# Performance work log

Hardware: AMD Instinct MI355X
Metric: run time of the kernel (lower is better)

Reference implementation:

```python
import jax, jax.numpy as jnp
import numpy as np

D_MODEL = 1024
NHEAD = 16
DFF = 4096
B = 4
L = 1024
EPS = 1e-5


def _layernorm(x, g, b):
    mu = jnp.mean(x, axis=-1, keepdims=True)
    var = jnp.mean((x - mu) ** 2, axis=-1, keepdims=True)
    return (x - mu) * jax.lax.rsqrt(var + EPS) * g + b


def _mha(q, k, v, wq, bq, wk, bk, wv, bv, wo, bo, mask=None):
    # q: [B,Lq,D], k/v: [B,Lk,D]; weights stored as [D_in, D_out]
    Bq, Lq, D = q.shape
    depth = D // NHEAD

    def split(x):  # [B,L,D] -> [B,H,L,depth]
        return x.reshape(Bq, -1, NHEAD, depth).transpose(0, 2, 1, 3)

    Q = split(q @ wq + bq)
    K = split(k @ wk + bk)
    V = split(v @ wv + bv)
    logits = jnp.einsum('bhqd,bhkd->bhqk', Q, K) / (depth ** 0.5)
    if mask is not None:
        logits = jnp.where(mask, logits, jnp.asarray(-1e9, logits.dtype))
    w = jax.nn.softmax(logits, axis=-1)
    o = jnp.einsum('bhqk,bhkd->bhqd', w, V)
    o = o.transpose(0, 2, 1, 3).reshape(Bq, -1, D)
    return o @ wo + bo


def setup_inputs() -> dict:
    key = jax.random.key(0)
    ks = jax.random.split(key, 16)
    s = 0.02

    def w(k, shp):
        return jax.random.normal(k, shp, jnp.float32) * s

    d, f = D_MODEL, DFF
    inp = {
        'tgt': jax.random.normal(ks[0], (B, L, d), jnp.float32),
        'memory': jax.random.normal(ks[1], (B, L, d), jnp.float32),
        'tgt_mask': jnp.tril(jnp.ones((L, L), jnp.bool_)),
        # self-attention params
        'sa_wq': w(ks[2], (d, d)), 'sa_bq': jnp.zeros((d,), jnp.float32),
        'sa_wk': w(ks[3], (d, d)), 'sa_bk': jnp.zeros((d,), jnp.float32),
        'sa_wv': w(ks[4], (d, d)), 'sa_bv': jnp.zeros((d,), jnp.float32),
        'sa_wo': w(ks[5], (d, d)), 'sa_bo': jnp.zeros((d,), jnp.float32),
        # cross-attention params
        'ca_wq': w(ks[6], (d, d)), 'ca_bq': jnp.zeros((d,), jnp.float32),
        'ca_wk': w(ks[7], (d, d)), 'ca_bk': jnp.zeros((d,), jnp.float32),
        'ca_wv': w(ks[8], (d, d)), 'ca_bv': jnp.zeros((d,), jnp.float32),
        'ca_wo': w(ks[9], (d, d)), 'ca_bo': jnp.zeros((d,), jnp.float32),
        # FFN params
        'ffn_w1': w(ks[10], (d, f)), 'ffn_b1': jnp.zeros((f,), jnp.float32),
        'ffn_w2': w(ks[11], (f, d)), 'ffn_b2': jnp.zeros((d,), jnp.float32),
        # LayerNorm params
        'ln1_g': jnp.ones((d,), jnp.float32), 'ln1_b': jnp.zeros((d,), jnp.float32),
        'ln2_g': jnp.ones((d,), jnp.float32), 'ln2_b': jnp.zeros((d,), jnp.float32),
        'ln3_g': jnp.ones((d,), jnp.float32), 'ln3_b': jnp.zeros((d,), jnp.float32),
    }
    return inp


def reference(tgt, memory, tgt_mask,
              sa_wq, sa_bq, sa_wk, sa_bk, sa_wv, sa_bv, sa_wo, sa_bo,
              ca_wq, ca_bq, ca_wk, ca_bk, ca_wv, ca_bv, ca_wo, ca_bo,
              ffn_w1, ffn_b1, ffn_w2, ffn_b2,
              ln1_g, ln1_b, ln2_g, ln2_b, ln3_g, ln3_b):
    # merge_mask with key_padding_mask=None -> mask used directly, broadcast over B,H
    mask = tgt_mask[None, None, :, :]
    t2 = _mha(tgt, tgt, tgt, sa_wq, sa_bq, sa_wk, sa_bk, sa_wv, sa_bv, sa_wo, sa_bo, mask)
    x = _layernorm(tgt + t2, ln1_g, ln1_b)
    t2 = _mha(x, memory, memory, ca_wq, ca_bq, ca_wk, ca_bk, ca_wv, ca_bv, ca_wo, ca_bo, None)
    x = _layernorm(x + t2, ln2_g, ln2_b)
    t2 = jax.nn.relu(x @ ffn_w1 + ffn_b1) @ ffn_w2 + ffn_b2
    x = _layernorm(x + t2, ln3_g, ln3_b)
    return x
```

## Files before the change

kernel.cpp:

```cpp
#include <hip/hip_runtime.h>
#include <hip/hip_bf16.h>

typedef unsigned short u16;
typedef __attribute__((ext_vector_type(8))) short bf16x8;
typedef __attribute__((ext_vector_type(4))) float floatx4;

__device__ inline float u2f(unsigned u) { union { unsigned i; float f; } x; x.i = u; return x.f; }
__device__ inline float bflo(unsigned p) { return u2f(p << 16); }
__device__ inline float bfhi(unsigned p) { return u2f(p & 0xffff0000u); }
__device__ inline u16 f2bf(float f) {
    union { __hip_bfloat16 h; u16 u; } x;
    x.h = __float2bfloat16(f);
    return x.u;
}
__device__ inline unsigned pk2bf(float lo, float hi) {
    return ((unsigned)f2bf(hi) << 16) | f2bf(lo);
}

#define GLDS(g, l) __builtin_amdgcn_global_load_lds( \
    (const __attribute__((address_space(1))) void*)(g), \
    (__attribute__((address_space(3))) void*)(l), 16, 0, 0)

template<int EPI, int NF>
__global__ __launch_bounds__(256, 2) void gemm_mfma(
        const u16* __restrict__ A, const u16* __restrict__ Bt,
        const float* __restrict__ bias, const u16* __restrict__ res,
        void* __restrict__ Cv, u16* __restrict__ o1, u16* __restrict__ o2,
        int N, int K)
{
    constexpr int BN = NF * 32;
    constexpr int BLOADS = BN / 64;

    __shared__ u16 As0[128 * 32];
    __shared__ u16 Bs0[BN * 32];
    __shared__ u16 As1[128 * 32];
    __shared__ u16 Bs1[BN * 32];
    __shared__ u16 As2[128 * 32];
    __shared__ u16 Bs2[BN * 32];

    const int tid = threadIdx.x;
    const int lane = tid & 63, wv = tid >> 6;
    const int wr = wv >> 1, wc = wv & 1;

    const int gx = gridDim.x;
    const int nwg = gx * gridDim.y;
    const int bid0 = blockIdx.y * gx + blockIdx.x;
    const int nbid = (bid0 & 7) * (nwg >> 3) + (bid0 >> 3);
    const int bx = nbid % gx, by = nbid / gx;
    const int row0 = by * 128, col0 = bx * BN;

    const u16* pa[2];
    int ldst[2];
    #pragma unroll
    for (int i = 0; i < 2; ++i) {
        const int idx = i * 256 + tid;
        const int r = idx >> 2;
        const int kob = (idx & 3) << 4;
        const int sw = kob ^ (((r >> 1) & 3) << 4);
        pa[i] = A + (size_t)(row0 + r) * K + (sw >> 1);
        ldst[i] = idx * 8;
    }
    const u16* pb[BLOADS];
    int ldstB[BLOADS];
    #pragma unroll
    for (int i = 0; i < BLOADS; ++i) {
        const int idx = i * 256 + tid;
        const int r = idx >> 2;
        const int kob = (idx & 3) << 4;
        const int sw = kob ^ (((r >> 1) & 3) << 4);
        pb[i] = Bt + (size_t)(col0 + r) * K + (sw >> 1);
        ldstB[i] = idx * 8;
    }

    int offa[4], offb[NF];
    const int rsel = lane & 15, slot = lane >> 4;
    #pragma unroll
    for (int m = 0; m < 4; ++m) {
        const int ra = wr * 64 + m * 16 + rsel;
        offa[m] = ra * 32 + (((slot << 4) ^ (((ra >> 1) & 3) << 4)) >> 1);
    }
    #pragma unroll
    for (int n = 0; n < NF; ++n) {
        const int rb = wc * (NF * 16) + n * 16 + rsel;
        offb[n] = rb * 32 + (((slot << 4) ^ (((rb >> 1) & 3) << 4)) >> 1);
    }

    floatx4 acc[4][NF] = {};

#define STAGE(AA, BB, t) do {                                   \
        const int ko_ = (t) << 5;                               \
        GLDS(pa[0] + ko_, &AA[ldst[0]]);                        \
        GLDS(pa[1] + ko_, &AA[ldst[1]]);                        \
        _Pragma("unroll")                                       \
        for (int i = 0; i < BLOADS; ++i)                        \
            GLDS(pb[i] + ko_, &BB[ldstB[i]]);                   \
    } while (0)

#define COMPUTE(AA, BB) do {                                    \
        bf16x8 af[4], bfr[NF];                                  \
        _Pragma("unroll")                                       \
        for (int m = 0; m < 4; ++m) af[m] = *(const bf16x8*)&AA[offa[m]]; \
        _Pragma("unroll")                                       \
        for (int n = 0; n < NF; ++n) bfr[n] = *(const bf16x8*)&BB[offb[n]]; \
        _Pragma("unroll")                                       \
        for (int m = 0; m < 4; ++m)                             \
            _Pragma("unroll")                                   \
            for (int n = 0; n < NF; ++n)                        \
                acc[m][n] = __builtin_amdgcn_mfma_f32_16x16x32_bf16( \
                        af[m], bfr[n], acc[m][n], 0, 0, 0);     \
    } while (0)

#define PHASE(CA, CB, NA, NB, t) do {                           \
        if ((t) < nkt - 1) {                                    \
            if constexpr (NF == 4)                              \
                asm volatile("s_waitcnt vmcnt(4)" ::: "memory");\
            else                                                \
                asm volatile("s_waitcnt vmcnt(3)" ::: "memory");\
        } else {                                                \
            asm volatile("s_waitcnt vmcnt(0)" ::: "memory");    \
        }                                                       \
        __builtin_amdgcn_s_barrier();                           \
        __builtin_amdgcn_sched_barrier(0);                      \
        if ((t) + 2 < nkt) STAGE(NA, NB, (t) + 2);              \
        COMPUTE(CA, CB);                                        \
    } while (0)

    const int nkt = K >> 5;
    STAGE(As0, Bs0, 0);
    STAGE(As1, Bs1, 1);
    int t = 0;
    for (; t + 3 <= nkt; t += 3) {
        PHASE(As0, Bs0, As2, Bs2, t);
        PHASE(As1, Bs1, As0, Bs0, t + 1);
        PHASE(As2, Bs2, As1, Bs1, t + 2);
    }
    if (t < nkt)     PHASE(As0, Bs0, As2, Bs2, t);
    if (t + 1 < nkt) PHASE(As1, Bs1, As0, Bs0, t + 1);
#undef STAGE
#undef COMPUTE
#undef PHASE

    const int cr4 = (lane >> 4) * 4;
    const int cc = lane & 15;

    if (EPI == 5 || EPI == 6) {
        const int seg = col0 >> 10;
        const int vtseg = (EPI == 5) ? 2 : 1;
        u16* dst;
        if (EPI == 5) dst = (seg == 0) ? (u16*)Cv : (seg == 1 ? o1 : o2);
        else          dst = (seg == 0) ? (u16*)Cv : o1;

        if (seg == vtseg) {
            #pragma unroll
            for (int n = 0; n < NF; ++n) {
                const int col = col0 + wc * (NF * 16) + n * 16 + cc;
                const float bv = bias[col];
                const int vcol = col & 1023;
                const int h = vcol >> 6, d = vcol & 63;
                #pragma unroll
                for (int m = 0; m < 4; ++m) {
                    const int tk = row0 + wr * 64 + m * 16 + cr4;
                    const int b = tk >> 10;
                    ushort4 o4;
                    o4.x = f2bf(acc[m][n][0] + bv);
                    o4.y = f2bf(acc[m][n][1] + bv);
                    o4.z = f2bf(acc[m][n][2] + bv);
                    o4.w = f2bf(acc[m][n][3] + bv);
                    *(ushort4*)(dst +
                        (((size_t)(b * 16 + h) * 64 + d) * 1024 + (tk & 1023))) = o4;
                }
            }
        } else {
            #pragma unroll
            for (int n = 0; n < NF; ++n) {
                const int col = col0 + wc * (NF * 16) + n * 16 + cc;
                const float bv = bias[col];
                const int oc = col & 1023;
                #pragma unroll
                for (int m = 0; m < 4; ++m) {
                    const int rowb = row0 + wr * 64 + m * 16 + cr4;
                    #pragma unroll
                    for (int r = 0; r < 4; ++r)
                        dst[(size_t)(rowb + r) * 1024 + oc] = f2bf(acc[m][n][r] + bv);
                }
            }
        }
        return;
    }

    #pragma unroll
    for (int n = 0; n < NF; ++n) {
        const int col = col0 + wc * (NF * 16) + n * 16 + cc;
        const float bv = bias[col];
        #pragma unroll
        for (int m = 0; m < 4; ++m) {
            const int rowb = row0 + wr * 64 + m * 16 + cr4;
            #pragma unroll
            for (int r = 0; r < 4; ++r) {
                float v = acc[m][n][r] + bv;
                const size_t o = (size_t)(rowb + r) * N + col;
                if (EPI == 2 || EPI == 3) v += u2f((unsigned)res[o] << 16);
                if (EPI == 1) v = fmaxf(v, 0.f);
                if (EPI == 3) ((float*)Cv)[o] = v;
                else          ((u16*)Cv)[o] = f2bf(v);
            }
        }
    }
}

struct TrwB { const float* w[8]; u16* o[8]; };

__global__ __launch_bounds__(256) void trw8_kernel(TrwB p)
{
    __shared__ float ts[64][65];
    const int tid = threadIdx.x;
    const int n0 = blockIdx.x * 64, k0 = blockIdx.y * 64;
    const float* __restrict__ W = p.w[blockIdx.z];
    u16* __restrict__ Wt = p.o[blockIdx.z];
    const int tr = tid >> 4, tc4 = (tid & 15) * 4;
    #pragma unroll
    for (int i = 0; i < 4; ++i) {
        const float4 v = *(const float4*)(W + (size_t)(k0 + tr + i * 16) * 1024 + n0 + tc4);
        ts[tr + i * 16][tc4 + 0] = v.x;
        ts[tr + i * 16][tc4 + 1] = v.y;
        ts[tr + i * 16][tc4 + 2] = v.z;
        ts[tr + i * 16][tc4 + 3] = v.w;
    }
    __syncthreads();
    #pragma unroll
    for (int i = 0; i < 4; ++i) {
        const int nr = tr + i * 16;
        ushort4 o;
        o.x = f2bf(ts[tc4 + 0][nr]);
        o.y = f2bf(ts[tc4 + 1][nr]);
        o.z = f2bf(ts[tc4 + 2][nr]);
        o.w = f2bf(ts[tc4 + 3][nr]);
        *(ushort4*)(Wt + (size_t)(n0 + nr) * 1024 + k0 + tc4) = o;
    }
}

__global__ __launch_bounds__(256) void trw_kernel(
        const float* __restrict__ W, u16* __restrict__ Wt, int K, int N)
{
    __shared__ float ts[64][65];
    const int tid = threadIdx.x;
    const int n0 = blockIdx.x * 64, k0 = blockIdx.y * 64;
    const int tr = tid >> 4, tc4 = (tid & 15) * 4;
    #pragma unroll
    for (int i = 0; i < 4; ++i) {
        const float4 v = *(const float4*)(W + (size_t)(k0 + tr + i * 16) * N + n0 + tc4);
        ts[tr + i * 16][tc4 + 0] = v.x;
        ts[tr + i * 16][tc4 + 1] = v.y;
        ts[tr + i * 16][tc4 + 2] = v.z;
        ts[tr + i * 16][tc4 + 3] = v.w;
    }
    __syncthreads();
    #pragma unroll
    for (int i = 0; i < 4; ++i) {
        const int nr = tr + i * 16;
        ushort4 o;
        o.x = f2bf(ts[tc4 + 0][nr]);
        o.y = f2bf(ts[tc4 + 1][nr]);
        o.z = f2bf(ts[tc4 + 2][nr]);
        o.w = f2bf(ts[tc4 + 3][nr]);
        *(ushort4*)(Wt + (size_t)(n0 + nr) * K + k0 + tc4) = o;
    }
}

__global__ __launch_bounds__(256) void cvt_kernel(
        const float* __restrict__ in, u16* __restrict__ out, int n4)
{
    for (int i = blockIdx.x * 256 + threadIdx.x; i < n4; i += gridDim.x * 256) {
        const float4 v = ((const float4*)in)[i];
        ushort4 o;
        o.x = f2bf(v.x); o.y = f2bf(v.y); o.z = f2bf(v.z); o.w = f2bf(v.w);
        ((ushort4*)out)[i] = o;
    }
}

__global__ __launch_bounds__(256) void bcat_kernel(
        const float* __restrict__ b0, const float* __restrict__ b1,
        const float* __restrict__ b2, float* __restrict__ o, int n)
{
    const int i = blockIdx.x * 256 + threadIdx.x;
    if (i >= n) return;
    const float* s = (i < 1024) ? b0 : (i < 2048 ? b1 : b2);
    o[i] = s[i & 1023];
}

template<int CAUSAL>
__global__ __launch_bounds__(256) void fattn_mfma(
        const u16* __restrict__ Q, const u16* __restrict__ K,
        const u16* __restrict__ Vt, u16* __restrict__ O)
{
    __shared__ u16 Ks[64 * 64];
    __shared__ u16 Vs[64 * 64];
    __shared__ u16 Ps[64 * 64];

    const int tid = threadIdx.x;
    const int lane = tid & 63, wv = tid >> 6;
    const int g = lane >> 4, qx = lane & 15;
    const int bh = blockIdx.x;
    const int b = bh >> 4, h = bh & 15;
    const int qt = blockIdx.y, q0 = qt * 64;
    const float SCL = 0.18033688011f;

    const size_t qkbase = (size_t)b * (1024 * 1024) + (size_t)h * 64;
    const size_t vtbase = (size_t)bh * 64 * 1024;

    const int qr = wv * 16 + qx;
    const int qg = q0 + qr;
    const int swzq = (qr & 7) << 4;

    bf16x8 qf[2];
    #pragma unroll
    for (int ks = 0; ks < 2; ++ks)
        qf[ks] = *(const bf16x8*)(Q + qkbase + (size_t)qg * 1024 + ks * 32 + g * 8);

    const int r0 = tid >> 3, s0 = tid & 7;

    float m_i = -1e30f, l_i = 0.f;
    floatx4 o_acc[4] = {};

    const int ktmax = CAUSAL ? qt : 15;
    for (int kt = 0; kt <= ktmax; ++kt) {
        __syncthreads();
        #pragma unroll
        for (int i = 0; i < 2; ++i) {
            const int r = i * 32 + r0;
            const uint4 kv = *(const uint4*)(K + qkbase + (size_t)(kt * 64 + r) * 1024 + s0 * 8);
            *(uint4*)((char*)Ks + r * 128 + ((s0 ^ (r & 7)) << 4)) = kv;
            const uint4 vv = *(const uint4*)(Vt + vtbase + (size_t)r * 1024 + kt * 64 + s0 * 8);
            *(uint4*)((char*)Vs + r * 128 + ((s0 ^ (r & 7)) << 4)) = vv;
        }
        __syncthreads();

        floatx4 sa[4] = {};
        #pragma unroll
        for (int ks = 0; ks < 2; ++ks) {
            #pragma unroll
            for (int m = 0; m < 4; ++m) {
                const int rr = m * 16 + qx;
                const int sl = ks * 4 + g;
                const bf16x8 kf = *(const bf16x8*)((char*)Ks + rr * 128 + ((sl ^ (rr & 7)) << 4));
                sa[m] = __builtin_amdgcn_mfma_f32_16x16x32_bf16(kf, qf[ks], sa[m], 0, 0, 0);
            }
        }

        float p[4][4];
        float mx = -1e30f;
        #pragma unroll
        for (int m = 0; m < 4; ++m)
            #pragma unroll
            for (int r = 0; r < 4; ++r) {
                float v = sa[m][r] * SCL;
                if (CAUSAL && kt == qt) {
                    const int kl = m * 16 + g * 4 + r;
                    if (kl > qr) v = -1e30f;
                }
                p[m][r] = v;
                mx = fmaxf(mx, v);
            }
        mx = fmaxf(mx, __shfl_xor(mx, 16));
        mx = fmaxf(mx, __shfl_xor(mx, 32));

        const float mn = fmaxf(m_i, mx);
        const float al = exp2f(m_i - mn);
        m_i = mn;
        float rs = 0.f;
        #pragma unroll
        for (int m = 0; m < 4; ++m)
            #pragma unroll
            for (int r = 0; r < 4; ++r) { p[m][r] = exp2f(p[m][r] - mn); rs += p[m][r]; }
        rs += __shfl_xor(rs, 16);
        rs += __shfl_xor(rs, 32);
        l_i = l_i * al + rs;
        #pragma unroll
        for (int n = 0; n < 4; ++n) o_acc[n] *= al;

        #pragma unroll
        for (int m = 0; m < 4; ++m) {
            uint2 pk;
            pk.x = pk2bf(p[m][0], p[m][1]);
            pk.y = pk2bf(p[m][2], p[m][3]);
            *(uint2*)((char*)Ps + qr * 128 + ((m * 32 + g * 8) ^ swzq)) = pk;
        }

        #pragma unroll
        for (int ks2 = 0; ks2 < 2; ++ks2) {
            const bf16x8 pf = *(const bf16x8*)((char*)Ps + qr * 128 + ((ks2 * 64 + g * 16) ^ swzq));
            #pragma unroll
            for (int n = 0; n < 4; ++n) {
                const int rv = n * 16 + qx;
                const int sl = ks2 * 4 + g;
                const bf16x8 vf = *(const bf16x8*)((char*)Vs + rv * 128 + ((sl ^ (rv & 7)) << 4));
                o_acc[n] = __builtin_amdgcn_mfma_f32_16x16x32_bf16(vf, pf, o_acc[n], 0, 0, 0);
            }
        }
    }

    const float inv = 1.f / l_i;
    #pragma unroll
    for (int n = 0; n < 4; ++n) {
        uint2 ov;
        ov.x = pk2bf(o_acc[n][0] * inv, o_acc[n][1] * inv);
        ov.y = pk2bf(o_acc[n][2] * inv, o_acc[n][3] * inv);
        *(uint2*)((char*)Ps + qr * 128 + ((n * 32 + g * 8) ^ swzq)) = ov;
    }
    const int orow = wv * 16 + (lane >> 2);
    const int swzo = (orow & 7) << 4;
    #pragma unroll
    for (int i = 0; i < 2; ++i) {
        const int cb = ((lane & 3) * 2 + i) * 16;
        const uint4 ov = *(const uint4*)((char*)Ps + orow * 128 + (cb ^ swzo));
        *(uint4*)(O + qkbase + (size_t)(q0 + orow) * 1024 + cb / 2) = ov;
    }
}

__global__ __launch_bounds__(256) void ln_bf16_kernel(
        const u16* __restrict__ X, const float* __restrict__ g,
        const float* __restrict__ bta, u16* __restrict__ Y)
{
    __shared__ float red[4];
    const int row = blockIdx.x, tid = threadIdx.x;
    const int wave = tid >> 6, lane = tid & 63;

    const uint2 u = *(const uint2*)(X + (size_t)row * 1024 + tid * 4);
    const float x0 = bflo(u.x), x1 = bfhi(u.x), x2 = bflo(u.y), x3 = bfhi(u.y);

    float s = x0 + x1 + x2 + x3;
    #pragma unroll
    for (int off = 32; off; off >>= 1) s += __shfl_xor(s, off);
    if (lane == 0) red[wave] = s;
    __syncthreads();
    const float mu = (red[0] + red[1] + red[2] + red[3]) * (1.f / 1024.f);
    __syncthreads();

    const float d0 = x0 - mu, d1 = x1 - mu, d2 = x2 - mu, d3 = x3 - mu;
    float s2 = d0 * d0 + d1 * d1 + d2 * d2 + d3 * d3;
    #pragma unroll
    for (int off = 32; off; off >>= 1) s2 += __shfl_xor(s2, off);
    if (lane == 0) red[wave] = s2;
    __syncthreads();
    const float var = (red[0] + red[1] + red[2] + red[3]) * (1.f / 1024.f);
    const float rs = rsqrtf(var + 1e-5f);

    const float4 gg = ((const float4*)g)[tid];
    const float4 bb = ((const float4*)bta)[tid];
    ushort4 o;
    o.x = f2bf(d0 * rs * gg.x + bb.x);
    o.y = f2bf(d1 * rs * gg.y + bb.y);
    o.z = f2bf(d2 * rs * gg.z + bb.z);
    o.w = f2bf(d3 * rs * gg.w + bb.w);
    *(ushort4*)(Y + (size_t)row * 1024 + tid * 4) = o;
}

__global__ __launch_bounds__(256) void ln_kernel(
        const float* X, const float* __restrict__ g,
        const float* __restrict__ bta, float* Y)
{
    __shared__ float red[4];
    const int row = blockIdx.x;
    const int tid = threadIdx.x;
    const int wave = tid >> 6, lane = tid & 63;

    const float4 v = ((const float4*)(X + (size_t)row * 1024))[tid];

    float s = v.x + v.y + v.z + v.w;
    #pragma unroll
    for (int off = 32; off; off >>= 1) s += __shfl_xor(s, off);
    if (lane == 0) red[wave] = s;
    __syncthreads();
    const float mu = (red[0] + red[1] + red[2] + red[3]) * (1.f / 1024.f);
    __syncthreads();

    const float dx = v.x - mu, dy = v.y - mu, dz = v.z - mu, dw = v.w - mu;
    float s2 = dx * dx + dy * dy + dz * dz + dw * dw;
    #pragma unroll
    for (int off = 32; off; off >>= 1) s2 += __shfl_xor(s2, off);
    if (lane == 0) red[wave] = s2;
    __syncthreads();
    const float var = (red[0] + red[1] + red[2] + red[3]) * (1.f / 1024.f);
    const float rs = rsqrtf(var + 1e-5f);

    const float4 gg = ((const float4*)g)[tid];
    const float4 bb = ((const float4*)bta)[tid];
    float4 o;
    o.x = dx * rs * gg.x + bb.x;
    o.y = dy * rs * gg.y + bb.y;
    o.z = dz * rs * gg.z + bb.z;
    o.w = dw * rs * gg.w + bb.w;
    ((float4*)(Y + (size_t)row * 1024))[tid] = o;
}

extern "C" void kernel_launch(void* const* d_in, const int* in_sizes, int n_in,
                              void* d_out, int out_size, void* d_ws, size_t ws_size,
                              hipStream_t stream)
{
    const float* tgt    = (const float*)d_in[0];
    const float* mem    = (const float*)d_in[1];
    const float* sa_wq  = (const float*)d_in[3];
    const float* sa_bq  = (const float*)d_in[4];
    const float* sa_wk  = (const float*)d_in[5];
    const float* sa_bk  = (const float*)d_in[6];
    const float* sa_wv  = (const float*)d_in[7];
    const float* sa_bv  = (const float*)d_in[8];
    const float* sa_wo  = (const float*)d_in[9];
    const float* sa_bo  = (const float*)d_in[10];
    const float* ca_wq  = (const float*)d_in[11];
    const float* ca_bq  = (const float*)d_in[12];
    const float* ca_wk  = (const float*)d_in[13];
    const float* ca_bk  = (const float*)d_in[14];
    const float* ca_wv  = (const float*)d_in[15];
    const float* ca_bv  = (const float*)d_in[16];
    const float* ca_wo  = (const float*)d_in[17];
    const float* ca_bo  = (const float*)d_in[18];
    const float* ffn_w1 = (const float*)d_in[19];
    const float* ffn_b1 = (const float*)d_in[20];
    const float* ffn_w2 = (const float*)d_in[21];
    const float* ffn_b2 = (const float*)d_in[22];
    const float* ln1_g  = (const float*)d_in[23];
    const float* ln1_b  = (const float*)d_in[24];
    const float* ln2_g  = (const float*)d_in[25];
    const float* ln2_b  = (const float*)d_in[26];
    const float* ln3_g  = (const float*)d_in[27];
    const float* ln3_b  = (const float*)d_in[28];

    float* out = (float*)d_out;
    u16* wsb = (u16*)d_ws;
    const size_t M1 = 1024 * 1024;

    u16* Wsq = wsb + 0 * M1;
    u16* Wsk = wsb + 1 * M1;
    u16* Wsv = wsb + 2 * M1;
    u16* Wso = wsb + 3 * M1;
    u16* Wcq = wsb + 4 * M1;
    u16* Wck = wsb + 5 * M1;
    u16* Wcv = wsb + 6 * M1;
    u16* Wco = wsb + 7 * M1;
    u16* Wf1 = wsb + 8 * M1;
    u16* Wf2 = wsb + 12 * M1;

    u16* sl = wsb + 16 * M1;
    u16* s0 = sl + 0 * 4 * M1;
    u16* s1 = sl + 4 * M1;
    u16* s2 = sl + 8 * M1;
    u16* s3 = sl + 12 * M1;
    u16* s4 = sl + 16 * M1;
    u16* s5 = sl + 20 * M1;
    u16* H  = s0;

    float* biasQKV = (float*)(wsb + 40 * M1);
    float* biasKV  = biasQKV + 3072;

    const dim3 blk(256);
    const dim3 gqkv(24, 32);
    const dim3 gkv(16, 32);
    const dim3 g1(16, 32);
    const dim3 g4(32, 32);
    const dim3 ga(64, 16);
    const dim3 gln(4096);

    TrwB tb;
    tb.w[0] = sa_wq; tb.o[0] = Wsq;
    tb.w[1] = sa_wk; tb.o[1] = Wsk;
    tb.w[2] = sa_wv; tb.o[2] = Wsv;
    tb.w[3] = sa_wo; tb.o[3] = Wso;
    tb.w[4] = ca_wq; tb.o[4] = Wcq;
    tb.w[5] = ca_wk; tb.o[5] = Wck;
    tb.w[6] = ca_wv; tb.o[6] = Wcv;
    tb.w[7] = ca_wo; tb.o[7] = Wco;
    trw8_kernel<<<dim3(16, 16, 8), blk, 0, stream>>>(tb);
    trw_kernel<<<dim3(64, 16), blk, 0, stream>>>(ffn_w1, Wf1, 1024, 4096);
    trw_kernel<<<dim3(16, 64), blk, 0, stream>>>(ffn_w2, Wf2, 4096, 1024);
    bcat_kernel<<<12, blk, 0, stream>>>(sa_bq, sa_bk, sa_bv, biasQKV, 3072);
    bcat_kernel<<<8, blk, 0, stream>>>(ca_bk, ca_bv, ca_bv, biasKV, 2048);
    cvt_kernel<<<2048, blk, 0, stream>>>(tgt, s0, 1024 * 1024);
    cvt_kernel<<<2048, blk, 0, stream>>>(mem, s1, 1024 * 1024);

    gemm_mfma<5, 4><<<gqkv, blk, 0, stream>>>(s0, Wsq, biasQKV, nullptr,
                                              s2, s3, s4, 3072, 1024);
    fattn_mfma<1><<<ga, blk, 0, stream>>>(s2, s3, s4, s5);
    gemm_mfma<2, 2><<<g1, blk, 0, stream>>>(s5, Wso, sa_bo, s0, s2, nullptr, nullptr, 1024, 1024);
    ln_bf16_kernel<<<gln, blk, 0, stream>>>(s2, ln1_g, ln1_b, s3);

    gemm_mfma<0, 2><<<g1, blk, 0, stream>>>(s3, Wcq, ca_bq, nullptr, s2, nullptr, nullptr, 1024, 1024);
    gemm_mfma<6, 4><<<gkv, blk, 0, stream>>>(s1, Wck, biasKV, nullptr,
                                             s4, s5, nullptr, 2048, 1024);
    fattn_mfma<0><<<ga, blk, 0, stream>>>(s2, s4, s5, s0);
    gemm_mfma<2, 2><<<g1, blk, 0, stream>>>(s0, Wco, ca_bo, s3, s2, nullptr, nullptr, 1024, 1024);
    ln_bf16_kernel<<<gln, blk, 0, stream>>>(s2, ln2_g, ln2_b, s4);

    gemm_mfma<1, 4><<<g4, blk, 0, stream>>>(s4, Wf1, ffn_b1, nullptr, H, nullptr, nullptr, 4096, 1024);
    gemm_mfma<3, 2><<<g1, blk, 0, stream>>>(H, Wf2, ffn_b2, s4, out, nullptr, nullptr, 1024, 4096);
    ln_kernel<<<gln, blk, 0, stream>>>(out, ln3_g, ln3_b, out);
}
```

Before: 348.5 us.

## Split-K the FFN down-projection and fuse partial reduction into final LayerNorm

The second FFN GEMM (K=4096) is split into two K halves along a new grid z dimension, doubling the number of workgroups. Each half writes fp32 partial sums, the first one including the bias, into the output buffer and a reused workspace region. A new LayerNorm kernel then sums both partials and the bf16 residual before normalizing. The aim is better CU occupancy and load balance on the long-K GEMM, at the cost of an extra fp32 partial buffer write and read.

New measurement: 350.4 us. No clear change (+0.5%).

```diff
diff --git a/kernel.cpp b/kernel.cpp
--- a/kernel.cpp
+++ b/kernel.cpp
@@ -49,6 +49,9 @@
     const int bx = nbid % gx, by = nbid / gx;
     const int row0 = by * 128, col0 = bx * BN;
 
+    const int Keff = (EPI == 7) ? (K >> 1) : K;
+    const int k0off = (EPI == 7) ? blockIdx.z * Keff : 0;
+
     const u16* pa[2];
     int ldst[2];
     #pragma unroll
@@ -57,7 +60,7 @@
         const int r = idx >> 2;
         const int kob = (idx & 3) << 4;
         const int sw = kob ^ (((r >> 1) & 3) << 4);
-        pa[i] = A + (size_t)(row0 + r) * K + (sw >> 1);
+        pa[i] = A + (size_t)(row0 + r) * K + k0off + (sw >> 1);
         ldst[i] = idx * 8;
     }
     const u16* pb[BLOADS];
@@ -68,7 +71,7 @@
         const int r = idx >> 2;
         const int kob = (idx & 3) << 4;
         const int sw = kob ^ (((r >> 1) & 3) << 4);
-        pb[i] = Bt + (size_t)(col0 + r) * K + (sw >> 1);
+        pb[i] = Bt + (size_t)(col0 + r) * K + k0off + (sw >> 1);
         ldstB[i] = idx * 8;
     }
 
@@ -125,7 +128,7 @@
         COMPUTE(CA, CB);                                        \
     } while (0)
 
-    const int nkt = K >> 5;
+    const int nkt = Keff >> 5;
     STAGE(As0, Bs0, 0);
     STAGE(As1, Bs1, 1);
     int t = 0;
@@ -142,6 +145,24 @@
 
     const int cr4 = (lane >> 4) * 4;
     const int cc = lane & 15;
+
+    if (EPI == 7) {
+        float* dst = (blockIdx.z == 0) ? (float*)Cv : (float*)o1;
+        const bool addb = (blockIdx.z == 0);
+        #pragma unroll
+        for (int n = 0; n < NF; ++n) {
+            const int col = col0 + wc * (NF * 16) + n * 16 + cc;
+            const float bv = addb ? bias[col] : 0.f;
+            #pragma unroll
+            for (int m = 0; m < 4; ++m) {
+                const int rowb = row0 + wr * 64 + m * 16 + cr4;
+                #pragma unroll
+                for (int r = 0; r < 4; ++r)
+                    dst[(size_t)(rowb + r) * N + col] = acc[m][n][r] + bv;
+            }
+        }
+        return;
+    }
 
     if (EPI == 5 || EPI == 6) {
         const int seg = col0 >> 10;
@@ -199,10 +220,9 @@
             for (int r = 0; r < 4; ++r) {
                 float v = acc[m][n][r] + bv;
                 const size_t o = (size_t)(rowb + r) * N + col;
-                if (EPI == 2 || EPI == 3) v += u2f((unsigned)res[o] << 16);
+                if (EPI == 2) v += u2f((unsigned)res[o] << 16);
                 if (EPI == 1) v = fmaxf(v, 0.f);
-                if (EPI == 3) ((float*)Cv)[o] = v;
-                else          ((u16*)Cv)[o] = f2bf(v);
+                ((u16*)Cv)[o] = f2bf(v);
             }
         }
     }
@@ -455,8 +475,9 @@
     *(ushort4*)(Y + (size_t)row * 1024 + tid * 4) = o;
 }
 
-__global__ __launch_bounds__(256) void ln_kernel(
-        const float* X, const float* __restrict__ g,
+__global__ __launch_bounds__(256) void ln_res_kernel(
+        const float* X0, const float* __restrict__ X1,
+        const u16* __restrict__ res, const float* __restrict__ g,
         const float* __restrict__ bta, float* Y)
 {
     __shared__ float red[4];
@@ -464,9 +485,13 @@
     const int tid = threadIdx.x;
     const int wave = tid >> 6, lane = tid & 63;
 
-    const float4 v = ((const float4*)(X + (size_t)row * 1024))[tid];
-
-    float s = v.x + v.y + v.z + v.w;
+    const float4 v0 = ((const float4*)(X0 + (size_t)row * 1024))[tid];
+    const float4 v1 = ((const float4*)(X1 + (size_t)row * 1024))[tid];
+    const uint2 u = *(const uint2*)(res + (size_t)row * 1024 + tid * 4);
+    const float x0 = v0.x + v1.x + bflo(u.x), x1 = v0.y + v1.y + bfhi(u.x);
+    const float x2 = v0.z + v1.z + bflo(u.y), x3 = v0.w + v1.w + bfhi(u.y);
+
+    float s = x0 + x1 + x2 + x3;
     #pragma unroll
     for (int off = 32; off; off >>= 1) s += __shfl_xor(s, off);
     if (lane == 0) red[wave] = s;
@@ -474,8 +499,8 @@
     const float mu = (red[0] + red[1] + red[2] + red[3]) * (1.f / 1024.f);
     __syncthreads();
 
-    const float dx = v.x - mu, dy = v.y - mu, dz = v.z - mu, dw = v.w - mu;
-    float s2 = dx * dx + dy * dy + dz * dz + dw * dw;
+    const float d0 = x0 - mu, d1 = x1 - mu, d2 = x2 - mu, d3 = x3 - mu;
+    float s2 = d0 * d0 + d1 * d1 + d2 * d2 + d3 * d3;
     #pragma unroll
     for (int off = 32; off; off >>= 1) s2 += __shfl_xor(s2, off);
     if (lane == 0) red[wave] = s2;
@@ -486,10 +511,10 @@
     const float4 gg = ((const float4*)g)[tid];
     const float4 bb = ((const float4*)bta)[tid];
     float4 o;
-    o.x = dx * rs * gg.x + bb.x;
-    o.y = dy * rs * gg.y + bb.y;
-    o.z = dz * rs * gg.z + bb.z;
-    o.w = dw * rs * gg.w + bb.w;
+    o.x = d0 * rs * gg.x + bb.x;
+    o.y = d1 * rs * gg.y + bb.y;
+    o.z = d2 * rs * gg.z + bb.z;
+    o.w = d3 * rs * gg.w + bb.w;
     ((float4*)(Y + (size_t)row * 1024))[tid] = o;
 }
 
@@ -550,6 +575,8 @@
     u16* s5 = sl + 20 * M1;
     u16* H  = s0;
 
+    float* part1 = (float*)wsb;
+
     float* biasQKV = (float*)(wsb + 40 * M1);
     float* biasKV  = biasQKV + 3072;
 
@@ -558,6 +585,7 @@
     const dim3 gkv(16, 32);
     const dim3 g1(16, 32);
     const dim3 g4(32, 32);
+    const dim3 gf2(16, 32, 2);
     const dim3 ga(64, 16);
     const dim3 gln(4096);
 
@@ -592,6 +620,7 @@
     ln_bf16_kernel<<<gln, blk, 0, stream>>>(s2, ln2_g, ln2_b, s4);
 
     gemm_mfma<1, 4><<<g4, blk, 0, stream>>>(s4, Wf1, ffn_b1, nullptr, H, nullptr, nullptr, 4096, 1024);
-    gemm_mfma<3, 2><<<g1, blk, 0, stream>>>(H, Wf2, ffn_b2, s4, out, nullptr, nullptr, 1024, 4096);
-    ln_kernel<<<gln, blk, 0, stream>>>(out, ln3_g, ln3_b, out);
-}
+    gemm_mfma<7, 2><<<gf2, blk, 0, stream>>>(H, Wf2, ffn_b2, nullptr, out,
+                                             (u16*)part1, nullptr, 1024, 4096);
+    ln_res_kernel<<<gln, blk, 0, stream>>>(out, part1, s4, ln3_g, ln3_b, out);
+}
```
